# Optimization experiments

Measured on AMD Instinct MI355X. Metric: run time of the kernel, lower is better.

The kernel has to match this reference:

```python
import jax, jax.numpy as jnp
import numpy as np

B, S, D, H, M = 2, 2048, 1024, 16, 4096  # batch, seqlen, dim, n_heads, max_seq_len
HD = D // H  # head_dim = 64
EPS = 1e-5


def layernorm(x, g, b):
    mu = jnp.mean(x, axis=-1, keepdims=True)
    var = jnp.mean((x - mu) ** 2, axis=-1, keepdims=True)
    return (x - mu) * jax.lax.rsqrt(var + EPS) * g + b


def setup_inputs() -> dict:
    key = jax.random.key(0)
    ks = jax.random.split(key, 5)
    x = jax.random.normal(ks[0], (B, S, D), jnp.float32)
    # causal mask: >=0 -> keep, negative -> drop (forward does att *= mask >= 0)
    i = jnp.arange(S)
    mask = jnp.where(i[None, :] <= i[:, None], 0, -1).astype(jnp.int32)[None, None]
    w1 = jax.random.normal(ks[1], (4 * D, D), jnp.float32) * (D ** -0.5)
    b1 = jnp.zeros((4 * D,), jnp.float32)
    w2 = jax.random.normal(ks[2], (D, D), jnp.float32) * (D ** -0.5)
    b2 = jnp.zeros((D,), jnp.float32)
    g1 = jnp.ones((D,), jnp.float32)
    beta1 = jnp.zeros((D,), jnp.float32)
    g2 = jnp.ones((D,), jnp.float32)
    beta2 = jnp.zeros((D,), jnp.float32)
    pos_w = jax.random.normal(ks[3], (2 * M - 1,), jnp.float32) * 0.02
    return dict(x=x, mask=mask, w1=w1, b1=b1, w2=w2, b2=b2,
                g1=g1, beta1=beta1, g2=g2, beta2=beta2, pos_w=pos_w)


def reference(x, mask, w1, b1, w2, b2, g1, beta1, g2, beta2, pos_w):
    # f1 + silu, split into gate u and q/k/v
    h = jax.nn.silu(x @ w1.T + b1)                      # [B,S,4D]
    u, q, k, v = jnp.split(h, 4, axis=-1)
    to_heads = lambda t: t.reshape(B, S, H, HD).transpose(0, 2, 1, 3)  # [B,H,S,HD]
    u, q, k, v = map(to_heads, (u, q, k, v))
    # relative positional bias: bias[i,j] = pos_w[M-1 + (j - i)]
    rel = jnp.arange(S)[None, :] - jnp.arange(S)[:, None]
    bias = pos_w[M - 1 + rel]                           # [S,S]
    att = jax.nn.silu(jnp.einsum('bhqd,bhkd->bhqk', q, k) + bias)
    att = att * (mask >= 0)                             # [B,H,S,S]
    y = jnp.einsum('bhqk,bhkd->bhqd', att, v) * u
    y = y.transpose(0, 2, 1, 3).reshape(B, S, D)
    y = layernorm(y, g1, beta1)
    y = y @ w2.T + b2
    return layernorm(y + x, g2, beta2)
```

## Files before the change

kernel.cpp:

```cpp
#include <hip/hip_runtime.h>
#include <hip/hip_bf16.h>

#define BN   2
#define SEQ  2048
#define DIM  1024
#define NH   16
#define HD   64
#define D4   4096
#define MAXS 4096

using bf16 = __hip_bfloat16;
typedef __bf16 bf16x8 __attribute__((ext_vector_type(8)));
typedef float  f32x4  __attribute__((ext_vector_type(4)));

__device__ __forceinline__ float bf2f(bf16 v){ return __bfloat162float(v); }
__device__ __forceinline__ bf16  f2bf(float v){ return __float2bfloat16(v); }
__device__ __forceinline__ float silu_f(float v){
  const float e = __expf(-v);
  return v * __builtin_amdgcn_rcpf(1.f + e);
}

__device__ __forceinline__ void async16(void* lds, const void* g){
  __builtin_amdgcn_global_load_lds((const __attribute__((address_space(1))) void*)g,
                                   (__attribute__((address_space(3))) void*)lds, 16, 0, 0);
}
__device__ __forceinline__ f32x4 mfma16(bf16x8 a, bf16x8 b, f32x4 c){
  return __builtin_amdgcn_mfma_f32_16x16x32_bf16(a, b, c, 0, 0, 0);
}

__global__ __launch_bounds__(256) void f2bk3(
    const float* __restrict__ a, bf16* __restrict__ ao, int na,
    const float* __restrict__ b, bf16* __restrict__ bo, int nb,
    const float* __restrict__ c, bf16* __restrict__ co)
{
  int i = (blockIdx.x * 256 + threadIdx.x) * 4;
  const float* in; bf16* out;
  if (i < na){ in = a; out = ao; }
  else if (i < na + nb){ in = b; out = bo; i -= na; }
  else { in = c; out = co; i -= na + nb; }
  const float4 v = *(const float4*)(in + i);
  bf16 t0 = f2bf(v.x), t1 = f2bf(v.y), t2 = f2bf(v.z), t3 = f2bf(v.w);
  ushort4 o;
  o.x = *(unsigned short*)&t0; o.y = *(unsigned short*)&t1;
  o.z = *(unsigned short*)&t2; o.w = *(unsigned short*)&t3;
  *(ushort4*)((unsigned short*)out + i) = o;
}

template<int NTOT>
__global__ __launch_bounds__(256) void gemm_bt(
    const bf16* __restrict__ A, const bf16* __restrict__ W,
    const float* __restrict__ bias, bf16* __restrict__ outb, bf16* __restrict__ vt)
{
  constexpr int K = DIM;
  const int ntiles = NTOT / 128;
  const int m0 = (int)(blockIdx.x / ntiles) * 128;
  const int n0 = (int)(blockIdx.x % ntiles) * 128;
  __shared__ bf16 Al[128*32];
  __shared__ bf16 Bl[128*32];
  const int tid = threadIdx.x, wave = tid>>6, lane = tid&63;
  const int quad = lane>>4, l16 = lane&15;
  const int srow = lane>>2;
  const int sg   = ((lane&3) ^ ((lane>>3)&3)) * 8;
  const int wm = (wave>>1)*64, wn = (wave&1)*64;
  const int rkey = ((l16>>1)&3);

  f32x4 acc[4][4];
  #pragma unroll
  for (int i=0;i<4;i++)
    #pragma unroll
    for (int j=0;j<4;j++) acc[i][j] = (f32x4){0.f,0.f,0.f,0.f};

  const bf16* aB = A + m0*K;
  const bf16* wB = W + n0*K;

  for (int k0 = 0; k0 < K; k0 += 32){
    async16(&Al[wave*1024      ], aB + (wave*32      + srow)*K + k0 + sg);
    async16(&Al[wave*1024 + 512], aB + (wave*32 + 16 + srow)*K + k0 + sg);
    async16(&Bl[wave*1024      ], wB + (wave*32      + srow)*K + k0 + sg);
    async16(&Bl[wave*1024 + 512], wB + (wave*32 + 16 + srow)*K + k0 + sg);
    __syncthreads();
    bf16x8 af[4], bv[4];
    #pragma unroll
    for (int mt=0;mt<4;mt++) af[mt] = *(const bf16x8*)&Al[(wm+mt*16+l16)*32 + (quad ^ rkey)*8];
    #pragma unroll
    for (int nt=0;nt<4;nt++) bv[nt] = *(const bf16x8*)&Bl[(wn+nt*16+l16)*32 + (quad ^ rkey)*8];
    #pragma unroll
    for (int mt=0;mt<4;mt++)
      #pragma unroll
      for (int nt=0;nt<4;nt++)
        acc[mt][nt] = mfma16(af[mt], bv[nt], acc[mt][nt]);
    __syncthreads();
  }

  const bool vtile = (NTOT == 4096) && (n0 >= 3*DIM);
  if (!vtile){
    #pragma unroll
    for (int mt=0;mt<4;mt++){
      #pragma unroll
      for (int nt=0;nt<4;nt++){
        const int row = m0 + wm + mt*16 + quad*4;
        const int col = n0 + wn + nt*16 + l16;
        const float bvv = bias[col];
        #pragma unroll
        for (int r=0;r<4;r++){
          float v = silu_f(acc[mt][nt][r] + bvv);
          outb[(row+r)*NTOT + col] = f2bf(v);
        }
      }
    }
  } else {
    #pragma unroll
    for (int mt=0;mt<4;mt++){
      #pragma unroll
      for (int nt=0;nt<4;nt++){
        const int row = m0 + wm + mt*16 + quad*4;
        const int colg = n0 + wn + nt*16 + l16;
        const float bvv = bias[colg];
        const int col = colg - 3*DIM;
        const int hh = col >> 6, d = col & 63;
        const int bb = row >> 11, sl = row & 2047;
        ushort4 o;
        float v0 = silu_f(acc[mt][nt][0] + bvv);
        float v1 = silu_f(acc[mt][nt][1] + bvv);
        float v2 = silu_f(acc[mt][nt][2] + bvv);
        float v3 = silu_f(acc[mt][nt][3] + bvv);
        bf16 t0=f2bf(v0), t1=f2bf(v1), t2=f2bf(v2), t3=f2bf(v3);
        o.x=*(unsigned short*)&t0; o.y=*(unsigned short*)&t1;
        o.z=*(unsigned short*)&t2; o.w=*(unsigned short*)&t3;
        *(ushort4*)&vt[((bb*NH + hh)*HD + d)*SEQ + sl] = o;
      }
    }
  }
}

__global__ __launch_bounds__(256) void gemm_bt2(
    const bf16* __restrict__ A, const bf16* __restrict__ W,
    const float* __restrict__ bias, const float* __restrict__ resid,
    float* __restrict__ outf)
{
  constexpr int K = DIM, NTOT = DIM;
  const int ntiles = NTOT / 64;
  const int m0 = (int)(blockIdx.x / ntiles) * 128;
  const int n0 = (int)(blockIdx.x % ntiles) * 64;
  __shared__ bf16 Al[128*32];
  __shared__ bf16 Bl[64*32];
  const int tid = threadIdx.x, wave = tid>>6, lane = tid&63;
  const int quad = lane>>4, l16 = lane&15;
  const int srow = lane>>2;
  const int sg   = ((lane&3) ^ ((lane>>3)&3)) * 8;
  const int wm = wave*32;
  const int rkey = ((l16>>1)&3);

  f32x4 acc[2][4];
  #pragma unroll
  for (int i=0;i<2;i++)
    #pragma unroll
    for (int j=0;j<4;j++) acc[i][j] = (f32x4){0.f,0.f,0.f,0.f};

  const bf16* aB = A + m0*K;
  const bf16* wB = W + n0*K;

  for (int k0 = 0; k0 < K; k0 += 32){
    async16(&Al[wave*1024      ], aB + (wave*32      + srow)*K + k0 + sg);
    async16(&Al[wave*1024 + 512], aB + (wave*32 + 16 + srow)*K + k0 + sg);
    async16(&Bl[wave*512       ], wB + (wave*16      + srow)*K + k0 + sg);
    __syncthreads();
    bf16x8 af[2], bv[4];
    #pragma unroll
    for (int mt=0;mt<2;mt++) af[mt] = *(const bf16x8*)&Al[(wm+mt*16+l16)*32 + (quad ^ rkey)*8];
    #pragma unroll
    for (int nt=0;nt<4;nt++) bv[nt] = *(const bf16x8*)&Bl[(nt*16+l16)*32 + (quad ^ rkey)*8];
    #pragma unroll
    for (int mt=0;mt<2;mt++)
      #pragma unroll
      for (int nt=0;nt<4;nt++)
        acc[mt][nt] = mfma16(af[mt], bv[nt], acc[mt][nt]);
    __syncthreads();
  }

  #pragma unroll
  for (int mt=0;mt<2;mt++){
    #pragma unroll
    for (int nt=0;nt<4;nt++){
      const int row = m0 + wm + mt*16 + quad*4;
      const int col = n0 + nt*16 + l16;
      const float bvv = bias[col];
      #pragma unroll
      for (int r=0;r<4;r++){
        outf[(row+r)*NTOT + col] = acc[mt][nt][r] + bvv + resid[(row+r)*NTOT + col];
      }
    }
  }
}

__global__ __launch_bounds__(256) void attn(
    const bf16* __restrict__ h, const bf16* __restrict__ vt,
    const float* __restrict__ pw, float* __restrict__ yp0, float* __restrict__ yp1)
{
  const int bid  = blockIdx.x;
  const int xcd  = bid & 7;
  const int idx  = bid >> 3;
  const int g    = ((idx >> 5) << 3) | xcd;
  const int slot = idx & 31;
  const int p    = slot >> 1;
  const int ksp  = slot & 1;
  const int hh = g & 15, b = g >> 4;
  float* __restrict__ yp = ksp ? yp1 : yp0;

  __shared__ bf16 Kl[64*64];
  __shared__ bf16 Vl[64*64];
  __shared__ bf16 Pl[4][16*72];
  __shared__ float pwl[256];

  const int tid = threadIdx.x, wave = tid>>6, lane = tid&63;
  const int quad = lane>>4, l16 = lane&15;
  const int r8 = lane>>3;
  const int g8 = ((lane&7) ^ r8) * 8;

  const bf16* kgb = h + b*SEQ*D4 + 2*DIM + hh*HD;
  const bf16* vgb = vt + (b*NH + hh)*HD*SEQ;

  #pragma unroll
  for (int pass = 0; pass < 2; ++pass){
    const int qt = pass ? (31 - p) : p;
    const int q0 = qt * 64;

    const bf16* qbase = h + (b*SEQ + q0 + wave*16 + l16)*D4 + DIM + hh*HD;
    bf16x8 qf[2];
    qf[0] = *(const bf16x8*)(qbase + quad*8);
    qf[1] = *(const bf16x8*)(qbase + 32 + quad*8);

    f32x4 oacc[4];
    #pragma unroll
    for (int nt=0;nt<4;nt++) oacc[nt] = (f32x4){0.f,0.f,0.f,0.f};

    for (int ic = ksp; ic <= qt; ic += 2){
      const int k0 = ic * 64;
      #pragma unroll
      for (int t=0;t<2;t++)
        async16(&Kl[(wave*16 + t*8)*64], kgb + (k0 + wave*16 + t*8 + r8)*D4 + g8);
      #pragma unroll
      for (int t=0;t<2;t++)
        async16(&Vl[(wave*16 + t*8)*64], vgb + (wave*16 + t*8 + r8)*SEQ + k0 + g8);
      if (wave == 0) async16(&pwl[0], pw + (MAXS-1 + k0 - q0 - 63) + lane*4);
      __syncthreads();

      f32x4 sacc[4];
      #pragma unroll
      for (int nt=0;nt<4;nt++) sacc[nt] = (f32x4){0.f,0.f,0.f,0.f};
      #pragma unroll
      for (int ks=0;ks<2;ks++){
        #pragma unroll
        for (int nt=0;nt<4;nt++){
          bf16x8 kf = *(const bf16x8*)&Kl[(nt*16 + l16)*64 + ((ks*4 + quad) ^ (l16&7))*8];
          sacc[nt] = mfma16(kf, qf[ks], sacc[nt]);
        }
      }

      const int dq = q0 - k0;
      const int qrl = wave*16 + l16;
      #pragma unroll
      for (int nt=0;nt<4;nt++){
        const int kb = nt*16 + quad*4;
        bf16 tb[4];
        #pragma unroll
        for (int r=0;r<4;r++){
          const int d = kb + r - qrl;
          const float bias = pwl[d + 63];
          const float sv = silu_f(sacc[nt][r] + bias);
          tb[r] = f2bf((d <= dq) ? sv : 0.f);
        }
        ushort4 o;
        o.x=*(unsigned short*)&tb[0]; o.y=*(unsigned short*)&tb[1];
        o.z=*(unsigned short*)&tb[2]; o.w=*(unsigned short*)&tb[3];
        *(ushort4*)&Pl[wave][l16*72 + kb] = o;
      }

      #pragma unroll
      for (int ks=0;ks<2;ks++){
        bf16x8 pf = *(const bf16x8*)&Pl[wave][l16*72 + ks*32 + quad*8];
        #pragma unroll
        for (int nt=0;nt<4;nt++){
          bf16x8 vf = *(const bf16x8*)&Vl[(nt*16 + l16)*64 + ((ks*4 + quad) ^ (l16&7))*8];
          oacc[nt] = mfma16(pf, vf, oacc[nt]);
        }
      }
      __syncthreads();
    }

    const int qrow = q0 + wave*16 + quad*4;
    #pragma unroll
    for (int nt=0;nt<4;nt++){
      const int c = hh*HD + nt*16 + l16;
      #pragma unroll
      for (int r=0;r<4;r++){
        yp[(b*SEQ + qrow + r)*DIM + c] = oacc[nt][r];
      }
    }
  }
}

__global__ __launch_bounds__(256) void lnorm_fuse(
    const float* __restrict__ ya, const float* __restrict__ yb,
    const bf16* __restrict__ h, const float* __restrict__ g,
    const float* __restrict__ be, bf16* __restrict__ out)
{
  const int row = blockIdx.x;
  const int tid = threadIdx.x, wave = tid>>6, lane = tid&63;
  const int c0 = tid*4;
  const float4 a  = *(const float4*)(ya + row*DIM + c0);
  const float4 bb = *(const float4*)(yb + row*DIM + c0);
  const ushort4 uu = *(const ushort4*)((const unsigned short*)h + row*D4 + c0);
  float v[4];
  {
    bf16 u0,u1,u2,u3;
    *(unsigned short*)&u0 = uu.x; *(unsigned short*)&u1 = uu.y;
    *(unsigned short*)&u2 = uu.z; *(unsigned short*)&u3 = uu.w;
    v[0] = (a.x + bb.x) * bf2f(u0);
    v[1] = (a.y + bb.y) * bf2f(u1);
    v[2] = (a.z + bb.z) * bf2f(u2);
    v[3] = (a.w + bb.w) * bf2f(u3);
  }
  float s = 0.f, ss = 0.f;
  #pragma unroll
  for (int j=0;j<4;j++){ s += v[j]; ss += v[j]*v[j]; }
  #pragma unroll
  for (int off=32; off>0; off>>=1){
    s  += __shfl_down(s, off);
    ss += __shfl_down(ss, off);
  }
  __shared__ float red[8];
  if (lane==0){ red[wave] = s; red[4+wave] = ss; }
  __syncthreads();
  s  = red[0]+red[1]+red[2]+red[3];
  ss = red[4]+red[5]+red[6]+red[7];
  const float mu   = s * (1.f/DIM);
  const float var  = ss * (1.f/DIM) - mu*mu;
  const float rstd = rsqrtf(var + 1e-5f);
  #pragma unroll
  for (int j=0;j<4;j++){
    const int c = c0 + j;
    out[row*DIM + c] = f2bf((v[j]-mu)*rstd*g[c] + be[c]);
  }
}

__global__ __launch_bounds__(256) void lnorm2k(const float* __restrict__ in,
    const float* __restrict__ g, const float* __restrict__ be, float* __restrict__ out)
{
  const int row = blockIdx.x;
  const int tid = threadIdx.x, wave = tid>>6, lane = tid&63;
  const int c0 = tid*4;
  const float4 a = *(const float4*)(in + row*DIM + c0);
  float v[4] = {a.x, a.y, a.z, a.w};
  float s = 0.f, ss = 0.f;
  #pragma unroll
  for (int j=0;j<4;j++){ s += v[j]; ss += v[j]*v[j]; }
  #pragma unroll
  for (int off=32; off>0; off>>=1){
    s  += __shfl_down(s, off);
    ss += __shfl_down(ss, off);
  }
  __shared__ float red[8];
  if (lane==0){ red[wave] = s; red[4+wave] = ss; }
  __syncthreads();
  s  = red[0]+red[1]+red[2]+red[3];
  ss = red[4]+red[5]+red[6]+red[7];
  const float mu   = s * (1.f/DIM);
  const float var  = ss * (1.f/DIM) - mu*mu;
  const float rstd = rsqrtf(var + 1e-5f);
  #pragma unroll
  for (int j=0;j<4;j++){
    const int c = c0 + j;
    out[row*DIM + c] = (v[j]-mu)*rstd*g[c] + be[c];
  }
}

extern "C" void kernel_launch(void* const* d_in, const int* in_sizes, int n_in,
                              void* d_out, int out_size, void* d_ws, size_t ws_size,
                              hipStream_t stream)
{
  const float* x   = (const float*)d_in[0];
  const float* w1  = (const float*)d_in[2];
  const float* b1  = (const float*)d_in[3];
  const float* w2  = (const float*)d_in[4];
  const float* b2  = (const float*)d_in[5];
  const float* g1  = (const float*)d_in[6];
  const float* be1 = (const float*)d_in[7];
  const float* g2  = (const float*)d_in[8];
  const float* be2 = (const float*)d_in[9];
  const float* pw  = (const float*)d_in[10];

  char* ws = (char*)d_ws;
  bf16*  h   = (bf16*)(ws);
  bf16*  vt  = (bf16*)(ws + (32u<<20));
  float* y0  = (float*)(ws + (40u<<20));
  float* y1  = (float*)(ws + (56u<<20));
  bf16*  xb  = (bf16*)(ws + (72u<<20));
  bf16*  w1b = (bf16*)(ws + (80u<<20));
  bf16*  w2b = (bf16*)(ws + (88u<<20));
  bf16*  l1  = (bf16*)(ws + (32u<<20));
  float* z   = (float*)(ws + (40u<<20));

  const int NX  = BN*SEQ*DIM;
  const int NW1 = 4*DIM*DIM;
  const int NW2 = DIM*DIM;
  f2bk3<<<dim3((NX+NW1+NW2)/1024), dim3(256), 0, stream>>>(x, xb, NX, w1, w1b, NW1, w2, w2b);

  gemm_bt<4096><<<dim3(1024), dim3(256), 0, stream>>>(xb, w1b, b1, h, vt);
  attn<<<dim3(1024), dim3(256), 0, stream>>>(h, vt, pw, y0, y1);
  lnorm_fuse<<<dim3(4096), dim3(256), 0, stream>>>(y0, y1, h, g1, be1, l1);
  gemm_bt2<<<dim3(512), dim3(256), 0, stream>>>(l1, w2b, b2, x, z);
  lnorm2k<<<dim3(4096), dim3(256), 0, stream>>>(z, g2, be2, (float*)d_out);
}
```

Before: 246.2 us.

## Restructure attention to 128-row query tiles with direct global K/V loads

Each attention block now handles a 128-row query tile, with each wave computing two 16-row m-tiles, and the grid is halved. K and V fragments are read straight from global memory instead of being staged in LDS, which removes the per-chunk __syncthreads barriers. The whole needed positional-bias window is preloaded into LDS once per block, and the causal mask is skipped on fully unmasked tiles. Each K/V fragment is reused across two m-tiles, but there is no LDS sharing of K/V between waves, so global/L2 traffic may rise, and the smaller grid lowers parallelism.

After: 266.5 us. 1.08x slower.

```diff
diff --git a/kernel.cpp b/kernel.cpp
--- a/kernel.cpp
+++ b/kernel.cpp
@@ -200,101 +200,118 @@
   const int bid  = blockIdx.x;
   const int xcd  = bid & 7;
   const int idx  = bid >> 3;
-  const int g    = ((idx >> 5) << 3) | xcd;
-  const int slot = idx & 31;
+  const int g    = ((idx >> 4) << 3) | xcd;
+  const int slot = idx & 15;
   const int p    = slot >> 1;
   const int ksp  = slot & 1;
   const int hh = g & 15, b = g >> 4;
   float* __restrict__ yp = ksp ? yp1 : yp0;
 
-  __shared__ bf16 Kl[64*64];
-  __shared__ bf16 Vl[64*64];
-  __shared__ bf16 Pl[4][16*72];
-  __shared__ float pwl[256];
+  __shared__ float pwl[3072];
+  __shared__ bf16 Pl[4][32*72];
 
   const int tid = threadIdx.x, wave = tid>>6, lane = tid&63;
   const int quad = lane>>4, l16 = lane&15;
-  const int r8 = lane>>3;
-  const int g8 = ((lane&7) ^ r8) * 8;
+
+  #pragma unroll
+  for (int rr=0;rr<3;rr++)
+    async16(&pwl[(rr*256 + tid)*4], pw + 2048 + (rr*256 + tid)*4);
+  __syncthreads();
 
   const bf16* kgb = h + b*SEQ*D4 + 2*DIM + hh*HD;
   const bf16* vgb = vt + (b*NH + hh)*HD*SEQ;
 
   #pragma unroll
   for (int pass = 0; pass < 2; ++pass){
-    const int qt = pass ? (31 - p) : p;
-    const int q0 = qt * 64;
-
-    const bf16* qbase = h + (b*SEQ + q0 + wave*16 + l16)*D4 + DIM + hh*HD;
-    bf16x8 qf[2];
-    qf[0] = *(const bf16x8*)(qbase + quad*8);
-    qf[1] = *(const bf16x8*)(qbase + 32 + quad*8);
-
-    f32x4 oacc[4];
-    #pragma unroll
-    for (int nt=0;nt<4;nt++) oacc[nt] = (f32x4){0.f,0.f,0.f,0.f};
-
-    for (int ic = ksp; ic <= qt; ic += 2){
+    const int qt = pass ? (15 - p) : p;
+    const int q0 = qt * 128;
+
+    bf16x8 qf[2][2];
+    #pragma unroll
+    for (int mt=0;mt<2;mt++){
+      const bf16* qb = h + (b*SEQ + q0 + wave*32 + mt*16 + l16)*D4 + DIM + hh*HD;
+      qf[mt][0] = *(const bf16x8*)(qb + quad*8);
+      qf[mt][1] = *(const bf16x8*)(qb + 32 + quad*8);
+    }
+
+    f32x4 oacc[2][4];
+    #pragma unroll
+    for (int mt=0;mt<2;mt++)
+      #pragma unroll
+      for (int nt=0;nt<4;nt++) oacc[mt][nt] = (f32x4){0.f,0.f,0.f,0.f};
+
+    const int nch = 2*(qt+1);
+    for (int ic = ksp; ic < nch; ic += 2){
       const int k0 = ic * 64;
-      #pragma unroll
-      for (int t=0;t<2;t++)
-        async16(&Kl[(wave*16 + t*8)*64], kgb + (k0 + wave*16 + t*8 + r8)*D4 + g8);
-      #pragma unroll
-      for (int t=0;t<2;t++)
-        async16(&Vl[(wave*16 + t*8)*64], vgb + (wave*16 + t*8 + r8)*SEQ + k0 + g8);
-      if (wave == 0) async16(&pwl[0], pw + (MAXS-1 + k0 - q0 - 63) + lane*4);
-      __syncthreads();
-
-      f32x4 sacc[4];
-      #pragma unroll
-      for (int nt=0;nt<4;nt++) sacc[nt] = (f32x4){0.f,0.f,0.f,0.f};
+
+      f32x4 sacc[2][4];
+      #pragma unroll
+      for (int mt=0;mt<2;mt++)
+        #pragma unroll
+        for (int nt=0;nt<4;nt++) sacc[mt][nt] = (f32x4){0.f,0.f,0.f,0.f};
       #pragma unroll
       for (int ks=0;ks<2;ks++){
         #pragma unroll
         for (int nt=0;nt<4;nt++){
-          bf16x8 kf = *(const bf16x8*)&Kl[(nt*16 + l16)*64 + ((ks*4 + quad) ^ (l16&7))*8];
-          sacc[nt] = mfma16(kf, qf[ks], sacc[nt]);
+          bf16x8 kf = *(const bf16x8*)(kgb + (k0 + nt*16 + l16)*D4 + ks*32 + quad*8);
+          sacc[0][nt] = mfma16(kf, qf[0][ks], sacc[0][nt]);
+          sacc[1][nt] = mfma16(kf, qf[1][ks], sacc[1][nt]);
         }
       }
 
-      const int dq = q0 - k0;
-      const int qrl = wave*16 + l16;
+      #pragma unroll
+      for (int mt=0;mt<2;mt++){
+        const int ibase = q0 + wave*32 + mt*16 + l16;
+        const bool need_mask = (k0 + 63 > q0 + wave*32 + mt*16);
+        #pragma unroll
+        for (int nt=0;nt<4;nt++){
+          const int jbase = k0 + nt*16 + quad*4;
+          const int dd0 = jbase - ibase;
+          bf16 tb[4];
+          if (need_mask){
+            #pragma unroll
+            for (int r=0;r<4;r++){
+              const float bias = pwl[dd0 + r + 2047];
+              const float sv = silu_f(sacc[mt][nt][r] + bias);
+              tb[r] = f2bf((dd0 + r <= 0) ? sv : 0.f);
+            }
+          } else {
+            #pragma unroll
+            for (int r=0;r<4;r++){
+              const float bias = pwl[dd0 + r + 2047];
+              tb[r] = f2bf(silu_f(sacc[mt][nt][r] + bias));
+            }
+          }
+          ushort4 o;
+          o.x=*(unsigned short*)&tb[0]; o.y=*(unsigned short*)&tb[1];
+          o.z=*(unsigned short*)&tb[2]; o.w=*(unsigned short*)&tb[3];
+          *(ushort4*)&Pl[wave][(mt*16 + l16)*72 + nt*16 + quad*4] = o;
+        }
+      }
+
+      #pragma unroll
+      for (int ks=0;ks<2;ks++){
+        bf16x8 pf0 = *(const bf16x8*)&Pl[wave][(l16     )*72 + ks*32 + quad*8];
+        bf16x8 pf1 = *(const bf16x8*)&Pl[wave][(16 + l16)*72 + ks*32 + quad*8];
+        #pragma unroll
+        for (int nt=0;nt<4;nt++){
+          bf16x8 vf = *(const bf16x8*)(vgb + (nt*16 + l16)*SEQ + k0 + ks*32 + quad*8);
+          oacc[0][nt] = mfma16(pf0, vf, oacc[0][nt]);
+          oacc[1][nt] = mfma16(pf1, vf, oacc[1][nt]);
+        }
+      }
+    }
+
+    #pragma unroll
+    for (int mt=0;mt<2;mt++){
+      const int qrow = q0 + wave*32 + mt*16 + quad*4;
       #pragma unroll
       for (int nt=0;nt<4;nt++){
-        const int kb = nt*16 + quad*4;
-        bf16 tb[4];
+        const int c = hh*HD + nt*16 + l16;
         #pragma unroll
         for (int r=0;r<4;r++){
-          const int d = kb + r - qrl;
-          const float bias = pwl[d + 63];
-          const float sv = silu_f(sacc[nt][r] + bias);
-          tb[r] = f2bf((d <= dq) ? sv : 0.f);
+          yp[(b*SEQ + qrow + r)*DIM + c] = oacc[mt][nt][r];
         }
-        ushort4 o;
-        o.x=*(unsigned short*)&tb[0]; o.y=*(unsigned short*)&tb[1];
-        o.z=*(unsigned short*)&tb[2]; o.w=*(unsigned short*)&tb[3];
-        *(ushort4*)&Pl[wave][l16*72 + kb] = o;
-      }
-
-      #pragma unroll
-      for (int ks=0;ks<2;ks++){
-        bf16x8 pf = *(const bf16x8*)&Pl[wave][l16*72 + ks*32 + quad*8];
-        #pragma unroll
-        for (int nt=0;nt<4;nt++){
-          bf16x8 vf = *(const bf16x8*)&Vl[(nt*16 + l16)*64 + ((ks*4 + quad) ^ (l16&7))*8];
-          oacc[nt] = mfma16(pf, vf, oacc[nt]);
-        }
-      }
-      __syncthreads();
-    }
-
-    const int qrow = q0 + wave*16 + quad*4;
-    #pragma unroll
-    for (int nt=0;nt<4;nt++){
-      const int c = hh*HD + nt*16 + l16;
-      #pragma unroll
-      for (int r=0;r<4;r++){
-        yp[(b*SEQ + qrow + r)*DIM + c] = oacc[nt][r];
       }
     }
   }
@@ -407,7 +424,7 @@
   f2bk3<<<dim3((NX+NW1+NW2)/1024), dim3(256), 0, stream>>>(x, xb, NX, w1, w1b, NW1, w2, w2b);
 
   gemm_bt<4096><<<dim3(1024), dim3(256), 0, stream>>>(xb, w1b, b1, h, vt);
-  attn<<<dim3(1024), dim3(256), 0, stream>>>(h, vt, pw, y0, y1);
+  attn<<<dim3(512), dim3(256), 0, stream>>>(h, vt, pw, y0, y1);
   lnorm_fuse<<<dim3(4096), dim3(256), 0, stream>>>(y0, y1, h, g1, be1, l1);
   gemm_bt2<<<dim3(512), dim3(256), 0, stream>>>(l1, w2b, b2, x, z);
   lnorm2k<<<dim3(4096), dim3(256), 0, stream>>>(z, g2, be2, (float*)d_out);
```
